# Kernel optimization log

Hardware: AMD Instinct MI355X
Metric: run time of the kernel (lower is better)

Reference implementation:

```python
import jax, jax.numpy as jnp
import numpy as np

N_ATOMS = 3
HIDDEN = 256
N_PAIRS = N_ATOMS * (N_ATOMS - 1) // 2  # 3
BATCH = 500000


def setup_inputs() -> dict:
    key = jax.random.key(0)
    ks = jax.random.split(key, 8)
    s1 = 1.0 / np.sqrt(N_PAIRS)
    s2 = 1.0 / np.sqrt(HIDDEN)
    return {
        "x": jax.random.normal(ks[0], (BATCH, N_ATOMS * 3), dtype=jnp.float32),
        "W1": jax.random.normal(ks[1], (N_PAIRS, HIDDEN), dtype=jnp.float32) * s1,
        "b1": jnp.zeros((HIDDEN,), dtype=jnp.float32),
        "W2": jax.random.normal(ks[2], (HIDDEN, HIDDEN), dtype=jnp.float32) * s2,
        "b2": jnp.zeros((HIDDEN,), dtype=jnp.float32),
        "W3": jax.random.normal(ks[3], (HIDDEN, 3), dtype=jnp.float32) * s2,
        "b3": jnp.zeros((3,), dtype=jnp.float32),
    }


def reference(x, W1, b1, W2, b2, W3, b3):
    # --- pairwise bond lengths (vectorized over batch) ---
    pts = x.reshape(-1, N_ATOMS, 3)                       # [B, n_atoms, 3]
    iu, ju = np.triu_indices(N_ATOMS, 1)                  # static index arrays
    diff = pts[:, iu, :] - pts[:, ju, :]                  # [B, n_pairs, 3]
    r = jnp.sqrt(jnp.sum(diff * diff, axis=-1))           # [B, n_pairs]
    # --- MLP: Dense->relu->Dense->relu->Dense (sizes=[256,256,3]) ---
    h = jax.nn.relu(r @ W1 + b1)                          # [B, 256]
    h = jax.nn.relu(h @ W2 + b2)                          # [B, 256]
    w = h @ W3 + b3                                       # [B, 3] -> (w00, w11, w01)
    # --- analytic eigenvalues of symmetric 2x2 [[w00,w01],[w01,w11]] ---
    # eigh returns ascending order: mean -/+ radius
    m = 0.5 * (w[:, 0] + w[:, 1])
    d = 0.5 * (w[:, 0] - w[:, 1])
    rad = jnp.sqrt(d * d + w[:, 2] * w[:, 2])
    return jnp.stack([m - rad, m + rad], axis=-1)         # [B, 2]
```

## Files before the change

kernel.cpp:

```cpp
#include <hip/hip_runtime.h>
#include <hip/hip_bf16.h>
#include <stdint.h>

typedef __attribute__((ext_vector_type(8)))  short short8;
typedef __attribute__((ext_vector_type(16))) float f32x16;

#define NCHUNK 15625
#define NBLK 256
#define NTHR 512
#define NWAVE_TOT (NBLK * 8)

#define SW(v) ((((v) & ~12u)) | (((v) & 4u) << 1) | (((v) & 8u) >> 1))

#define A2_OFF   0
#define A1_OFF   131072
#define Z_OFF    135168
#define A3_OFF   135184
#define SCR_OFF  136720
#define LDS_TOTAL 153104

__device__ __forceinline__ uint32_t cvtpk(float lo, float hi) {
    uint32_t r;
    asm("v_cvt_pk_bf16_f32 %0, %1, %2" : "=v"(r) : "v"(lo), "v"(hi));
    return r;
}

__global__ __launch_bounds__(NTHR, 2) void fused_kernel(
    const float* __restrict__ x,  const float* __restrict__ W1,
    const float* __restrict__ b1, const float* __restrict__ W2,
    const float* __restrict__ b2, const float* __restrict__ W3,
    const float* __restrict__ b3, float* __restrict__ out)
{
    extern __shared__ char smem[];
    uint4* frag4 = (uint4*)(smem + A2_OFF);
    float* scrf  = (float*)(smem + SCR_OFF);
    uint4* scr4  = (uint4*)(smem + SCR_OFF);

    const int tid = threadIdx.x;
    const int l   = tid & 63;
    const int hi  = l >> 5;
    const int c   = l & 31;

    {
        int fr = tid >> 6, l2 = tid & 63;
        if (l2 < 32) {
            int row = fr * 32 + l2;
            uint4 v;
            v.x = cvtpk(W1[row], W1[256 + row]);
            v.y = cvtpk(W1[512 + row], b1[row]);
            v.z = 0; v.w = 0;
            ((uint4*)(smem + A1_OFF))[fr * 32 + l2] = v;
        }
        if (tid == 511) ((uint4*)(smem + Z_OFF))[0] = make_uint4(0, 0, 0, 0);
        if (tid < 96) {
            int fr3 = tid / 6, rem = tid % 6, hi2 = rem / 3, c2 = rem % 3;
            int kb = 16 * fr3 + 8 * hi2;
            uint4 v;
            v.x = cvtpk(W3[(kb + 0) * 3 + c2], W3[(kb + 1) * 3 + c2]);
            v.y = cvtpk(W3[(kb + 2) * 3 + c2], W3[(kb + 3) * 3 + c2]);
            v.z = cvtpk(W3[(kb + 4) * 3 + c2], W3[(kb + 5) * 3 + c2]);
            v.w = cvtpk(W3[(kb + 6) * 3 + c2], W3[(kb + 7) * 3 + c2]);
            ((uint4*)(smem + A3_OFF))[fr3 * 6 + rem] = v;
        }
    }
    const uint4* gw2 = (const uint4*)W2;
    for (int kt = 0; kt < 16; ++kt) {
        __syncthreads();
        scr4[tid]       = gw2[kt * 1024 + tid];
        scr4[tid + 512] = gw2[kt * 1024 + 512 + tid];
        __syncthreads();
        int mt = tid >> 6, l2 = tid & 63, hi2 = l2 >> 5, c2 = l2 & 31;
        int col = 32 * mt + (int)SW((unsigned)c2);
        float f[8];
#pragma unroll
        for (int j = 0; j < 8; ++j) {
            int lrow = 8 * (j >> 2) + 4 * hi2 + (j & 3);
            f[j] = scrf[lrow * 256 + col];
        }
        uint4 v;
        v.x = cvtpk(f[0], f[1]); v.y = cvtpk(f[2], f[3]);
        v.z = cvtpk(f[4], f[5]); v.w = cvtpk(f[6], f[7]);
        frag4[(kt * 8 + mt) * 64 + l2] = v;
    }
    __syncthreads();

    const f32x16 Z = {0,0,0,0,0,0,0,0,0,0,0,0,0,0,0,0};
    uint32_t b2pk[8];
#pragma unroll
    for (int mt = 0; mt < 8; ++mt)
        b2pk[mt] = hi ? 0u : cvtpk(b2[32 * mt + (int)SW((unsigned)c)], 0.0f);
    union { short8 s8; uint32_t u[4]; } bB;
    bB.u[0] = hi ? 0u : 0x3F80u; bB.u[1] = 0; bB.u[2] = 0; bB.u[3] = 0;
    const short8 biasB = bB.s8;
    const float b30 = b3[0], b31 = b3[1], b32 = b3[2];

    const int a1step = hi ? 0 : 512;
    const int a1base = hi ? Z_OFF : (A1_OFF + c * 16);
    const int a3step = (c < 3) ? 96 : 0;
    const int a3base = (c < 3) ? (A3_OFF + (hi * 3 + c) * 16) : Z_OFF;

    const int gwave = blockIdx.x * 8 + (tid >> 6);

    float xb[9], xn[9];
    {
        const float* xp = x + (size_t)(gwave * 32 + c) * 9;
#pragma unroll
        for (int j = 0; j < 9; ++j) xb[j] = xp[j];
    }

    for (int chunk = gwave; chunk < NCHUNK; chunk += NWAVE_TOT) {
        {
            int nxt = chunk + NWAVE_TOT;
            const float* xpn = x + (size_t)(((nxt < NCHUNK) ? nxt : chunk) * 32 + c) * 9;
#pragma unroll
            for (int j = 0; j < 9; ++j) xn[j] = xpn[j];
        }
        float d0 = xb[0] - xb[3], d1 = xb[1] - xb[4], d2 = xb[2] - xb[5];
        float e0 = xb[0] - xb[6], e1 = xb[1] - xb[7], e2 = xb[2] - xb[8];
        float f0 = xb[3] - xb[6], f1 = xb[4] - xb[7], f2 = xb[5] - xb[8];
        float q0 = sqrtf(fmaf(d0, d0, fmaf(d1, d1, d2 * d2)));
        float q1 = sqrtf(fmaf(e0, e0, fmaf(e1, e1, e2 * e2)));
        float q2 = sqrtf(fmaf(f0, f0, fmaf(f1, f1, f2 * f2)));

        union { short8 s8; uint32_t u[4]; } qf;
        qf.u[0] = hi ? 0u : cvtpk(q0, q1);
        qf.u[1] = hi ? 0u : cvtpk(q2, 1.0f);
        qf.u[2] = 0; qf.u[3] = 0;
        const short8 qfrag = qf.s8;

        f32x16 acc[8];
#pragma unroll
        for (int mt = 0; mt < 8; ++mt) {
            union { short8 s8; uint32_t u[4]; } bA;
            bA.u[0] = b2pk[mt]; bA.u[1] = 0; bA.u[2] = 0; bA.u[3] = 0;
            acc[mt] = __builtin_amdgcn_mfma_f32_32x32x16_bf16(bA.s8, biasB, Z, 0, 0, 0);
        }

#pragma unroll
        for (int tau = 0; tau < 8; ++tau) {
            short8 a1 = *(const short8*)(smem + a1base + tau * a1step);
            f32x16 d1v = __builtin_amdgcn_mfma_f32_32x32x16_bf16(a1, qfrag, Z, 0, 0, 0);
#pragma unroll
            for (int p = 0; p < 2; ++p) {
                const int kt = 2 * tau + p;
                union { short8 s8; uint32_t u[4]; } pk;
#pragma unroll
                for (int w = 0; w < 4; ++w)
                    pk.u[w] = cvtpk(fmaxf(d1v[8 * p + 2 * w], 0.0f),
                                    fmaxf(d1v[8 * p + 2 * w + 1], 0.0f));
                const short8 bfr = pk.s8;
#pragma unroll
                for (int mt = 0; mt < 8; ++mt) {
                    short8 a2 = *(const short8*)(smem + (size_t)(kt * 8 + mt) * 1024 + l * 16);
                    acc[mt] = __builtin_amdgcn_mfma_f32_32x32x16_bf16(a2, bfr, acc[mt], 0, 0, 0);
                }
            }
        }

        f32x16 d3 = Z;
#pragma unroll
        for (int kt3 = 0; kt3 < 16; ++kt3) {
            const int mt = kt3 >> 1, p = kt3 & 1;
            union { short8 s8; uint32_t u[4]; } pk;
#pragma unroll
            for (int w = 0; w < 4; ++w)
                pk.u[w] = cvtpk(fmaxf(acc[mt][8 * p + 2 * w], 0.0f),
                                fmaxf(acc[mt][8 * p + 2 * w + 1], 0.0f));
            short8 a3 = *(const short8*)(smem + a3base + kt3 * a3step);
            d3 = __builtin_amdgcn_mfma_f32_32x32x16_bf16(a3, pk.s8, d3, 0, 0, 0);
        }

        if (hi == 0) {
            float w0 = d3[0] + b30, w1v = d3[1] + b31, wc = d3[2] + b32;
            float mm = 0.5f * (w0 + w1v), dd = 0.5f * (w0 - w1v);
            float rad = sqrtf(fmaf(dd, dd, wc * wc));
            *(float2*)(out + (size_t)(chunk * 32 + c) * 2) = make_float2(mm - rad, mm + rad);
        }

#pragma unroll
        for (int j = 0; j < 9; ++j) xb[j] = xn[j];
    }
}

extern "C" void kernel_launch(void* const* d_in, const int* in_sizes, int n_in,
                              void* d_out, int out_size, void* d_ws, size_t ws_size,
                              hipStream_t stream) {
    const float* x  = (const float*)d_in[0];
    const float* W1 = (const float*)d_in[1];
    const float* b1 = (const float*)d_in[2];
    const float* W2 = (const float*)d_in[3];
    const float* b2 = (const float*)d_in[4];
    const float* W3 = (const float*)d_in[5];
    const float* b3 = (const float*)d_in[6];
    float* out = (float*)d_out;

    (void)d_ws; (void)ws_size;

    (void)hipFuncSetAttribute((const void*)fused_kernel,
                              hipFuncAttributeMaxDynamicSharedMemorySize, LDS_TOTAL);

    fused_kernel<<<NBLK, NTHR, LDS_TOTAL, stream>>>(x, W1, b1, W2, b2, W3, b3, out);
}
```

Before: 145.0 us.

## Process two 32-row tiles per wave to reuse W2 fragments across tiles

Each wave now handles 64 rows per chunk (two N-tiles), so each W2 fragment read from LDS feeds two MFMAs. The hidden-layer accumulators are split into four passes of two M-tiles each, and the third layer is folded incrementally into each pass to keep register pressure bounded. The layer-1 MFMAs are recomputed for every pass, which adds extra work. Rows past the end are clamped on load and masked on store. This cuts LDS traffic per MFMA but doubles the x prefetch registers and may change occupancy and load balance (7813 chunks over 2048 waves).

```diff
diff --git a/kernel.cpp b/kernel.cpp
--- a/kernel.cpp
+++ b/kernel.cpp
@@ -5,7 +5,8 @@
 typedef __attribute__((ext_vector_type(8)))  short short8;
 typedef __attribute__((ext_vector_type(16))) float f32x16;
 
-#define NCHUNK 15625
+#define NROWS 500000
+#define NCHUNK 7813
 #define NBLK 256
 #define NTHR 512
 #define NWAVE_TOT (NBLK * 8)
@@ -101,84 +102,123 @@
 
     const int gwave = blockIdx.x * 8 + (tid >> 6);
 
-    float xb[9], xn[9];
+    float xb[18], xn[18];
     {
-        const float* xp = x + (size_t)(gwave * 32 + c) * 9;
-#pragma unroll
-        for (int j = 0; j < 9; ++j) xb[j] = xp[j];
+        int r0 = gwave * 64 + c;
+#pragma unroll
+        for (int nt = 0; nt < 2; ++nt) {
+            int row = r0 + nt * 32; row = row < NROWS ? row : NROWS - 1;
+            const float* xp = x + (size_t)row * 9;
+#pragma unroll
+            for (int j = 0; j < 9; ++j) xb[nt * 9 + j] = xp[j];
+        }
     }
 
     for (int chunk = gwave; chunk < NCHUNK; chunk += NWAVE_TOT) {
         {
-            int nxt = chunk + NWAVE_TOT;
-            const float* xpn = x + (size_t)(((nxt < NCHUNK) ? nxt : chunk) * 32 + c) * 9;
-#pragma unroll
-            for (int j = 0; j < 9; ++j) xn[j] = xpn[j];
-        }
-        float d0 = xb[0] - xb[3], d1 = xb[1] - xb[4], d2 = xb[2] - xb[5];
-        float e0 = xb[0] - xb[6], e1 = xb[1] - xb[7], e2 = xb[2] - xb[8];
-        float f0 = xb[3] - xb[6], f1 = xb[4] - xb[7], f2 = xb[5] - xb[8];
-        float q0 = sqrtf(fmaf(d0, d0, fmaf(d1, d1, d2 * d2)));
-        float q1 = sqrtf(fmaf(e0, e0, fmaf(e1, e1, e2 * e2)));
-        float q2 = sqrtf(fmaf(f0, f0, fmaf(f1, f1, f2 * f2)));
-
-        union { short8 s8; uint32_t u[4]; } qf;
-        qf.u[0] = hi ? 0u : cvtpk(q0, q1);
-        qf.u[1] = hi ? 0u : cvtpk(q2, 1.0f);
-        qf.u[2] = 0; qf.u[3] = 0;
-        const short8 qfrag = qf.s8;
-
-        f32x16 acc[8];
-#pragma unroll
-        for (int mt = 0; mt < 8; ++mt) {
-            union { short8 s8; uint32_t u[4]; } bA;
-            bA.u[0] = b2pk[mt]; bA.u[1] = 0; bA.u[2] = 0; bA.u[3] = 0;
-            acc[mt] = __builtin_amdgcn_mfma_f32_32x32x16_bf16(bA.s8, biasB, Z, 0, 0, 0);
-        }
-
-#pragma unroll
-        for (int tau = 0; tau < 8; ++tau) {
-            short8 a1 = *(const short8*)(smem + a1base + tau * a1step);
-            f32x16 d1v = __builtin_amdgcn_mfma_f32_32x32x16_bf16(a1, qfrag, Z, 0, 0, 0);
-#pragma unroll
-            for (int p = 0; p < 2; ++p) {
-                const int kt = 2 * tau + p;
-                union { short8 s8; uint32_t u[4]; } pk;
-#pragma unroll
-                for (int w = 0; w < 4; ++w)
-                    pk.u[w] = cvtpk(fmaxf(d1v[8 * p + 2 * w], 0.0f),
-                                    fmaxf(d1v[8 * p + 2 * w + 1], 0.0f));
-                const short8 bfr = pk.s8;
-#pragma unroll
-                for (int mt = 0; mt < 8; ++mt) {
-                    short8 a2 = *(const short8*)(smem + (size_t)(kt * 8 + mt) * 1024 + l * 16);
-                    acc[mt] = __builtin_amdgcn_mfma_f32_32x32x16_bf16(a2, bfr, acc[mt], 0, 0, 0);
+            int nxt = chunk + NWAVE_TOT; if (nxt >= NCHUNK) nxt = chunk;
+            int r0 = nxt * 64 + c;
+#pragma unroll
+            for (int nt = 0; nt < 2; ++nt) {
+                int row = r0 + nt * 32; row = row < NROWS ? row : NROWS - 1;
+                const float* xp = x + (size_t)row * 9;
+#pragma unroll
+                for (int j = 0; j < 9; ++j) xn[nt * 9 + j] = xp[j];
+            }
+        }
+
+        short8 qfrag[2];
+#pragma unroll
+        for (int nt = 0; nt < 2; ++nt) {
+            const float* xp = xb + nt * 9;
+            float d0 = xp[0] - xp[3], d1 = xp[1] - xp[4], d2 = xp[2] - xp[5];
+            float e0 = xp[0] - xp[6], e1 = xp[1] - xp[7], e2 = xp[2] - xp[8];
+            float f0 = xp[3] - xp[6], f1 = xp[4] - xp[7], f2 = xp[5] - xp[8];
+            float q0 = sqrtf(fmaf(d0, d0, fmaf(d1, d1, d2 * d2)));
+            float q1 = sqrtf(fmaf(e0, e0, fmaf(e1, e1, e2 * e2)));
+            float q2 = sqrtf(fmaf(f0, f0, fmaf(f1, f1, f2 * f2)));
+            union { short8 s8; uint32_t u[4]; } qf;
+            qf.u[0] = hi ? 0u : cvtpk(q0, q1);
+            qf.u[1] = hi ? 0u : cvtpk(q2, 1.0f);
+            qf.u[2] = 0; qf.u[3] = 0;
+            qfrag[nt] = qf.s8;
+        }
+
+        f32x16 d3[2] = {Z, Z};
+
+#pragma unroll
+        for (int P = 0; P < 4; ++P) {
+            f32x16 acc[2][2];
+#pragma unroll
+            for (int m2 = 0; m2 < 2; ++m2) {
+                union { short8 s8; uint32_t u[4]; } bA;
+                bA.u[0] = b2pk[2 * P + m2]; bA.u[1] = 0; bA.u[2] = 0; bA.u[3] = 0;
+#pragma unroll
+                for (int nt = 0; nt < 2; ++nt)
+                    acc[m2][nt] = __builtin_amdgcn_mfma_f32_32x32x16_bf16(bA.s8, biasB, Z, 0, 0, 0);
+            }
+#pragma unroll
+            for (int tau = 0; tau < 8; ++tau) {
+                short8 a1 = *(const short8*)(smem + a1base + tau * a1step);
+                f32x16 d1v[2];
+#pragma unroll
+                for (int nt = 0; nt < 2; ++nt)
+                    d1v[nt] = __builtin_amdgcn_mfma_f32_32x32x16_bf16(a1, qfrag[nt], Z, 0, 0, 0);
+#pragma unroll
+                for (int p = 0; p < 2; ++p) {
+                    const int kt = 2 * tau + p;
+                    short8 bfr[2];
+#pragma unroll
+                    for (int nt = 0; nt < 2; ++nt) {
+                        union { short8 s8; uint32_t u[4]; } pk;
+#pragma unroll
+                        for (int w = 0; w < 4; ++w)
+                            pk.u[w] = cvtpk(fmaxf(d1v[nt][8 * p + 2 * w], 0.0f),
+                                            fmaxf(d1v[nt][8 * p + 2 * w + 1], 0.0f));
+                        bfr[nt] = pk.s8;
+                    }
+#pragma unroll
+                    for (int m2 = 0; m2 < 2; ++m2) {
+                        short8 a2 = *(const short8*)(smem +
+                                     (size_t)((kt * 8 + 2 * P + m2) * 1024) + l * 16);
+#pragma unroll
+                        for (int nt = 0; nt < 2; ++nt)
+                            acc[m2][nt] = __builtin_amdgcn_mfma_f32_32x32x16_bf16(a2, bfr[nt], acc[m2][nt], 0, 0, 0);
+                    }
                 }
             }
-        }
-
-        f32x16 d3 = Z;
-#pragma unroll
-        for (int kt3 = 0; kt3 < 16; ++kt3) {
-            const int mt = kt3 >> 1, p = kt3 & 1;
-            union { short8 s8; uint32_t u[4]; } pk;
-#pragma unroll
-            for (int w = 0; w < 4; ++w)
-                pk.u[w] = cvtpk(fmaxf(acc[mt][8 * p + 2 * w], 0.0f),
-                                fmaxf(acc[mt][8 * p + 2 * w + 1], 0.0f));
-            short8 a3 = *(const short8*)(smem + a3base + kt3 * a3step);
-            d3 = __builtin_amdgcn_mfma_f32_32x32x16_bf16(a3, pk.s8, d3, 0, 0, 0);
+#pragma unroll
+            for (int i = 0; i < 4; ++i) {
+                const int kt3 = 4 * P + i;
+                const int m2 = i >> 1, p = i & 1;
+                short8 a3 = *(const short8*)(smem + a3base + kt3 * a3step);
+#pragma unroll
+                for (int nt = 0; nt < 2; ++nt) {
+                    union { short8 s8; uint32_t u[4]; } pk;
+#pragma unroll
+                    for (int w = 0; w < 4; ++w)
+                        pk.u[w] = cvtpk(fmaxf(acc[m2][nt][8 * p + 2 * w], 0.0f),
+                                        fmaxf(acc[m2][nt][8 * p + 2 * w + 1], 0.0f));
+                    d3[nt] = __builtin_amdgcn_mfma_f32_32x32x16_bf16(a3, pk.s8, d3[nt], 0, 0, 0);
+                }
+            }
         }
 
         if (hi == 0) {
-            float w0 = d3[0] + b30, w1v = d3[1] + b31, wc = d3[2] + b32;
-            float mm = 0.5f * (w0 + w1v), dd = 0.5f * (w0 - w1v);
-            float rad = sqrtf(fmaf(dd, dd, wc * wc));
-            *(float2*)(out + (size_t)(chunk * 32 + c) * 2) = make_float2(mm - rad, mm + rad);
-        }
-
-#pragma unroll
-        for (int j = 0; j < 9; ++j) xb[j] = xn[j];
+#pragma unroll
+            for (int nt = 0; nt < 2; ++nt) {
+                int row = chunk * 64 + nt * 32 + c;
+                if (row < NROWS) {
+                    float w0 = d3[nt][0] + b30, w1v = d3[nt][1] + b31, wc = d3[nt][2] + b32;
+                    float mm = 0.5f * (w0 + w1v), dd = 0.5f * (w0 - w1v);
+                    float rad = sqrtf(fmaf(dd, dd, wc * wc));
+                    *(float2*)(out + (size_t)row * 2) = make_float2(mm - rad, mm + rad);
+                }
+            }
+        }
+
+#pragma unroll
+        for (int j = 0; j < 18; ++j) xb[j] = xn[j];
     }
 }
 
```

New measurement: 162.2 us. 1.12x slower.
